# Optimization experiments

Hardware: AMD Instinct MI355X
Metric: run time of the kernel (lower is better)

Reference implementation:

```python
import jax, jax.numpy as jnp
from jax import lax
import numpy as np

STRIDE = 4
RADIUS = 0.2
NSAMPLE = 32
DENSITY_K = 16
INTRINSIC_DIM = 3
EPS = 1e-8
BN_EPS = 1e-5


def _cdist(a, b):
    # Euclidean pairwise distances: a (..., M, 3), b (..., N, 3) -> (..., M, N)
    d2 = ((a * a).sum(-1)[..., :, None] + (b * b).sum(-1)[..., None, :]
          - 2.0 * jnp.matmul(a, jnp.swapaxes(b, -1, -2)))
    return jnp.sqrt(jnp.maximum(d2, 1e-12))


def _fps(coords, n_samples):
    # iterative farthest point sampling: coords (B, N, 3) -> (B, n_samples) int32
    B, N, _ = coords.shape
    mean = coords.mean(axis=1, keepdims=True)
    farthest = jnp.argmax(((coords - mean) ** 2).sum(-1), axis=1)
    min_dist = jnp.full((B, N), jnp.inf, dtype=coords.dtype)

    def step(carry, _):
        md, far = carry
        centroid = jnp.take_along_axis(coords, far[:, None, None], axis=1)  # (B,1,3)
        d = ((coords - centroid) ** 2).sum(-1)
        md = jnp.minimum(md, d)
        return (md, jnp.argmax(md, axis=1)), far

    _, idxs = lax.scan(step, (min_dist, farthest), None, length=n_samples)
    return idxs.T  # (B, n_samples)


def _ball_query(q, s, radius, k):
    d = _cdist(q, s)  # (B, M, N)
    _, knn_idx = lax.top_k(-d, k)                 # k nearest fallback
    masked = jnp.where(d > radius, jnp.inf, d)
    neg_vals, m_idx = lax.top_k(-masked, k)       # k nearest within radius
    valid = jnp.isfinite(neg_vals)
    return jnp.where(valid, m_idx, knn_idx)


def _density_weights(gc):
    # gc: (B, M, K, 3) -> weights (B, M, K); kth-NN-distance based density weights
    K = gc.shape[2]
    d = _cdist(gc, gc)  # (B, M, K, K)
    d = jnp.where(jnp.eye(K, dtype=bool), jnp.inf, d)
    kk = min(max(DENSITY_K, 1), K - 1)
    kth = -lax.top_k(-d, kk)[0][..., -1]  # distance to kk-th neighbor, (B, M, K)
    raw = jnp.maximum(kth, EPS) ** INTRINSIC_DIM
    return raw / jnp.maximum(raw.sum(axis=-1, keepdims=True), EPS)


def _bn(x, g, b, axes):
    # training-mode batchnorm (biased variance), channel axis = 1
    mu = x.mean(axes, keepdims=True)
    var = x.var(axes, keepdims=True)
    shp = [1] * x.ndim
    shp[1] = -1
    return (x - mu) / jnp.sqrt(var + BN_EPS) * g.reshape(shp) + b.reshape(shp)


def setup_inputs() -> dict:
    key = jax.random.key(0)
    ks = jax.random.split(key, 5)
    B, N, C_in, C_out = 8, 4096, 64, 128
    mid = C_out // 2  # stride > 1 -> mid_channels = out_channels // 2
    coords = jax.random.uniform(ks[0], (B, N, 3), dtype=jnp.float32)
    feats = jax.random.normal(ks[1], (B, C_in, N), dtype=jnp.float32)
    W0 = jax.random.normal(ks[2], (mid, C_in + 3), dtype=jnp.float32) * 0.05
    W1 = jax.random.normal(ks[3], (C_out, mid), dtype=jnp.float32) * 0.05
    Ws = jax.random.normal(ks[4], (C_out, C_in), dtype=jnp.float32) * 0.05
    return {
        "coords": coords, "feats": feats,
        "W0": W0, "g0": jnp.ones((mid,), jnp.float32), "b0": jnp.zeros((mid,), jnp.float32),
        "W1": W1, "g1": jnp.ones((C_out,), jnp.float32), "b1": jnp.zeros((C_out,), jnp.float32),
        "Ws": Ws, "gs": jnp.ones((C_out,), jnp.float32), "bs": jnp.zeros((C_out,), jnp.float32),
    }


def reference(coords, feats, W0, g0, b0, W1, g1, b1, Ws, gs, bs):
    B, N, _ = coords.shape
    M = max(N // STRIDE, 1)
    sample_idx = _fps(coords, M)                               # (B, M)
    gather_pts = jax.vmap(lambda c, i: c[i])                   # (N,3)[idx]
    gather_fts = jax.vmap(lambda f, i: f[:, i])                # (C,N)[:,idx]
    sampled_coords = gather_pts(coords, sample_idx)            # (B, M, 3)
    gidx = _ball_query(sampled_coords, coords, RADIUS, NSAMPLE)  # (B, M, K)
    grouped_coords = gather_pts(coords, gidx)                  # (B, M, K, 3)
    rel = (grouped_coords - sampled_coords[:, :, None, :]) / max(RADIUS, 1e-8)
    grouped_feats = gather_fts(feats, gidx)                    # (B, C_in, M, K)
    x = jnp.concatenate([rel.transpose(0, 3, 1, 2), grouped_feats], axis=1)
    h = jax.nn.relu(_bn(jnp.einsum('oc,bcmk->bomk', W0, x), g0, b0, (0, 2, 3)))
    messages = jax.nn.relu(_bn(jnp.einsum('oc,bcmk->bomk', W1, h), g1, b1, (0, 2, 3)))
    weights = _density_weights(grouped_coords)                 # (B, M, K)
    reduced = (messages * weights[:, None, :, :]).sum(-1)      # (B, C_out, M)
    skip_in = gather_fts(feats, sample_idx)                    # (B, C_in, M)
    skip = _bn(jnp.einsum('oc,bcm->bom', Ws, skip_in), gs, bs, (0, 2))
    return sampled_coords, jax.nn.relu(reduced + skip)
```

## Files before the change

### kernel.cpp

```cpp
#include <hip/hip_runtime.h>
#include <hip/hip_bf16.h>
#include <cstdint>

#define DEV __device__ __forceinline__

constexpr int Bn   = 8;
constexpr int Nn   = 4096;
constexpr int Mn   = 1024;
constexpr int Kn   = 32;
constexpr int CIN  = 64;
constexpr int COUT = 128;

DEV float wave_max_f32(float x) {
#if __has_builtin(__builtin_amdgcn_update_dpp)
#define FSTEP(CTRL, RMASK)                                                      \
  {                                                                             \
    int o = __builtin_amdgcn_update_dpp(0, __float_as_int(x), CTRL, RMASK, 0xf, \
                                        false);                                 \
    x = fmaxf(x, __int_as_float(o));                                            \
  }
  FSTEP(0x111, 0xf)
  FSTEP(0x112, 0xf)
  FSTEP(0x114, 0xf)
  FSTEP(0x118, 0xf)
  FSTEP(0x142, 0xa)
  FSTEP(0x143, 0xc)
#undef FSTEP
#else
  for (int off = 1; off < 64; off <<= 1) x = fmaxf(x, __shfl_xor(x, off, 64));
#endif
  return x;
}

DEV unsigned long long grp8_max_u64(unsigned long long k) {
#if __has_builtin(__builtin_amdgcn_update_dpp)
#define USTEP(CTRL)                                                                    \
  {                                                                                    \
    unsigned int lo = (unsigned int)__builtin_amdgcn_update_dpp(                       \
        0, (int)(unsigned int)k, CTRL, 0xf, 0xf, false);                               \
    unsigned int hi = (unsigned int)__builtin_amdgcn_update_dpp(                       \
        0, (int)(unsigned int)(k >> 32), CTRL, 0xf, 0xf, false);                       \
    unsigned long long o = ((unsigned long long)hi << 32) | lo;                        \
    if (o > k) k = o;                                                                  \
  }
  USTEP(0x111)
  USTEP(0x112)
  USTEP(0x114)
#undef USTEP
#else
  for (int off = 1; off < 8; off <<= 1) {
    unsigned int lo = __shfl_xor((unsigned int)k, off, 64);
    unsigned int hi = __shfl_xor((unsigned int)(k >> 32), off, 64);
    unsigned long long o = ((unsigned long long)hi << 32) | lo;
    if (o > k) k = o;
  }
#endif
  return k;
}

DEV uint32_t fps_round8(const float v[8], int t, unsigned long long (*part)[8], int p) {
  float v4[4]; int j4[4];
#pragma unroll
  for (int i = 0; i < 4; ++i) {
    bool r = v[2 * i + 1] > v[2 * i];
    v4[i] = r ? v[2 * i + 1] : v[2 * i];
    j4[i] = r ? 2 * i + 1 : 2 * i;
  }
  float v2[2]; int j2[2];
#pragma unroll
  for (int i = 0; i < 2; ++i) {
    bool r = v4[2 * i + 1] > v4[2 * i];
    v2[i] = r ? v4[2 * i + 1] : v4[2 * i];
    j2[i] = r ? j4[2 * i + 1] : j4[2 * i];
  }
  bool rr = v2[1] > v2[0];
  float bv = rr ? v2[1] : v2[0];
  int bj = rr ? j2[1] : j2[0];

  unsigned long long mb0 = __ballot((bj & 1) != 0);
  unsigned long long mb1 = __ballot((bj & 2) != 0);
  unsigned long long mb2 = __ballot((bj & 4) != 0);
  float wl = wave_max_f32(bv);
  float wmax = __int_as_float(__builtin_amdgcn_readlane(__float_as_int(wl), 63));
  unsigned long long mask = __ballot(bv == wmax);
  int Ls = (int)__ffsll(mask) - 1;
  int bjw = (int)((mb0 >> Ls) & 1ull) | ((int)((mb1 >> Ls) & 1ull) << 1) |
            ((int)((mb2 >> Ls) & 1ull) << 2);
  uint32_t idx = 8u * (uint32_t)((t & ~63) + Ls) + (uint32_t)bjw;
  const int sl = p & 1;
  if ((t & 63) == 0)
    part[sl][t >> 6] = ((unsigned long long)__float_as_uint(wmax) << 12) |
                       (unsigned long long)(4095u - idx);
  __syncthreads();
  unsigned long long kk = part[sl][t & 7];
  kk = grp8_max_u64(kk);
  unsigned int lo = (unsigned int)__builtin_amdgcn_readlane((int)(unsigned int)kk, 7);
  return 4095u - (lo & 4095u);
}

__global__ __launch_bounds__(512, 1) void k_fused(const float* __restrict__ coords,
                                                  const float* __restrict__ feats,
                                                  float* __restrict__ featsT,
                                                  uint32_t* __restrict__ sidx,
                                                  float* __restrict__ outc) {
  __shared__ __align__(16) char smraw[Nn * 16];
  __shared__ unsigned long long part[2][8];
  __shared__ uint32_t farl[Mn];
  __shared__ float s_mean[4];
  const int t = threadIdx.x;

  if (blockIdx.x >= 8) {
    float (*tile)[65] = (float(*)[65])smraw;
    int bid = blockIdx.x - 8;
    int b = bid >> 6, n0 = (bid & 63) * 64;
    int lane = t & 63, grp = t >> 6;
    for (int r = 0; r < 8; ++r) {
      int c = grp + r * 8;
      tile[c][lane] = feats[((size_t)b * 64 + c) * 4096 + n0 + lane];
    }
    __syncthreads();
    for (int r = 0; r < 8; ++r) {
      int n = grp + r * 8;
      featsT[((size_t)b * 4096 + n0 + n) * 64 + lane] = tile[lane][n];
    }
    return;
  }

  float4* sp = (float4*)smraw;
  const int b = blockIdx.x;
  const float* cb = coords + (size_t)b * Nn * 3;
  for (int i = t; i < Nn; i += 512)
    sp[i] = make_float4(cb[3 * i], cb[3 * i + 1], cb[3 * i + 2], 0.f);
  __syncthreads();
  if (t == 0) {
    float ax = 0.f, ay = 0.f, az = 0.f;
    for (int i = 0; i < Nn; ++i) {
      float4 c = sp[i];
      ax = __fadd_rn(ax, c.x); ay = __fadd_rn(ay, c.y); az = __fadd_rn(az, c.z);
    }
    s_mean[0] = __fdiv_rn(ax, 4096.f);
    s_mean[1] = __fdiv_rn(ay, 4096.f);
    s_mean[2] = __fdiv_rn(az, 4096.f);
  }
  __syncthreads();

  float px[8], py[8], pz[8], md[8];
#pragma unroll
  for (int j = 0; j < 8; ++j) {
    float4 c = sp[8 * t + j];
    px[j] = c.x; py[j] = c.y; pz[j] = c.z;
    md[j] = __builtin_inff();
  }

  uint32_t far;
  {
    float mx = s_mean[0], my = s_mean[1], mz = s_mean[2];
    float tv[8];
#pragma unroll
    for (int j = 0; j < 8; ++j) {
      float dx = __fsub_rn(px[j], mx), dy = __fsub_rn(py[j], my), dz = __fsub_rn(pz[j], mz);
      tv[j] = __fadd_rn(__fadd_rn(__fmul_rn(dx, dx), __fmul_rn(dy, dy)), __fmul_rn(dz, dz));
    }
    far = fps_round8(tv, t, part, 0);
  }

  for (int p = 1; p < Mn; ++p) {
    if (t == 0) farl[p - 1] = far;
    float4 c = sp[far];
#pragma unroll
    for (int j = 0; j < 8; ++j) {
      float dx = __fsub_rn(px[j], c.x), dy = __fsub_rn(py[j], c.y), dz = __fsub_rn(pz[j], c.z);
      float d = __fadd_rn(__fadd_rn(__fmul_rn(dx, dx), __fmul_rn(dy, dy)), __fmul_rn(dz, dz));
      md[j] = fminf(md[j], d);
    }
    far = fps_round8(md, t, part, p);
  }
  if (t == 0) farl[Mn - 1] = far;
  __syncthreads();

  for (int i = t; i < Mn; i += 512) {
    uint32_t f = farl[i];
    sidx[b * Mn + i] = f;
    float4 c = sp[f];
    outc[(size_t)(b * Mn + i) * 3 + 0] = c.x;
    outc[(size_t)(b * Mn + i) * 3 + 1] = c.y;
    outc[(size_t)(b * Mn + i) * 3 + 2] = c.z;
  }
}

__global__ __launch_bounds__(256) void k_knn(const float* __restrict__ coords,
                                             const uint32_t* __restrict__ sidx,
                                             uint32_t* __restrict__ gidx,
                                             float* __restrict__ wts) {
  const int q = blockIdx.x;
  const int b = q >> 10;
  const int t = threadIdx.x;
  __shared__ unsigned long long keys[Nn + 2];
  __shared__ int s_cnt;
  __shared__ float s_q[4];
  __shared__ uint32_t s_sel[32];
  __shared__ float gx[32], gy[32], gz[32], g2[32];
  __shared__ float dmat[32 * 33];
  __shared__ float kth[32];
  __shared__ float s_raw[32];
  __shared__ float s_sum;

  if (t == 0) {
    uint32_t si = sidx[q];
    const float* c = &coords[((size_t)b * Nn + si) * 3];
    s_q[0] = c[0]; s_q[1] = c[1]; s_q[2] = c[2];
  }
  __syncthreads();
  float qx = s_q[0], qy = s_q[1], qz = s_q[2];
  float q2 = __fadd_rn(__fadd_rn(__fmul_rn(qx, qx), __fmul_rn(qy, qy)), __fmul_rn(qz, qz));
  const float* cb = coords + (size_t)b * Nn * 3;

  float thr = 0.04f;
  int cnt = 0;
  while (true) {
    if (t == 0) s_cnt = 0;
    __syncthreads();
    for (int j = 0; j < 16; ++j) {
      int i = t + 256 * j;
      float cx = cb[3 * i], cy = cb[3 * i + 1], cz = cb[3 * i + 2];
      float c2  = __fadd_rn(__fadd_rn(__fmul_rn(cx, cx), __fmul_rn(cy, cy)), __fmul_rn(cz, cz));
      float dot = __fadd_rn(__fadd_rn(__fmul_rn(qx, cx), __fmul_rn(qy, cy)), __fmul_rn(qz, cz));
      float d2  = __fsub_rn(__fadd_rn(q2, c2), __fmul_rn(2.f, dot));
      float d2c = fmaxf(d2, 1e-12f);
      bool pred = (d2c <= thr);
      unsigned long long mk = __ballot(pred);
      int base = 0;
      if ((t & 63) == 0 && mk) base = atomicAdd(&s_cnt, (int)__popcll(mk));
      base = __shfl(base, 0, 64);
      if (pred) {
        int pos = base + (int)__popcll(mk & ((1ull << (t & 63)) - 1ull));
        keys[pos] = ((unsigned long long)__float_as_uint(d2c) << 32) | (uint32_t)i;
      }
    }
    __syncthreads();
    cnt = s_cnt;
    if (cnt >= 32 || thr > 1.f) break;
    thr = (thr < 0.1f) ? 0.16f : 8.f;
    __syncthreads();
  }
  if (t == 0) { keys[cnt] = ~0ull; keys[cnt + 1] = ~0ull; }
  __syncthreads();
  int cnt2 = (cnt + 1) & ~1;
  for (int i = t; i < cnt; i += 256) {
    unsigned long long ki = keys[i];
    int r = 0;
    for (int j2 = 0; j2 < cnt2; j2 += 2) {
      unsigned long long a = keys[j2], c2 = keys[j2 + 1];
      r += (a < ki) + (c2 < ki);
    }
    if (r < 32) s_sel[r] = (uint32_t)ki;
  }
  __syncthreads();

  if (t < 32) {
    uint32_t gi = s_sel[t];
    gidx[(size_t)q * 32 + t] = gi;
    const float* c = &coords[((size_t)b * Nn + gi) * 3];
    float x = c[0], y = c[1], z = c[2];
    gx[t] = x; gy[t] = y; gz[t] = z;
    g2[t] = __fadd_rn(__fadd_rn(__fmul_rn(x, x), __fmul_rn(y, y)), __fmul_rn(z, z));
  }
  __syncthreads();
  for (int p = t; p < 1024; p += 256) {
    int i = p >> 5, jj = p & 31;
    float dot = __fadd_rn(__fadd_rn(__fmul_rn(gx[i], gx[jj]), __fmul_rn(gy[i], gy[jj])),
                          __fmul_rn(gz[i], gz[jj]));
    float d2 = __fsub_rn(__fadd_rn(g2[i], g2[jj]), __fmul_rn(2.f, dot));
    float dd = sqrtf(fmaxf(d2, 1e-12f));
    if (i == jj) dd = __builtin_inff();
    dmat[i * 33 + jj] = dd;
  }
  __syncthreads();
  for (int p = t; p < 1024; p += 256) {
    int i = p >> 5, jj = p & 31;
    float v = dmat[i * 33 + jj];
    int r = 0;
    for (int c = 0; c < 32; ++c) {
      float u = dmat[i * 33 + c];
      r += (u < v) || (u == v && c < jj);
    }
    if (r == 15) kth[i] = v;
  }
  __syncthreads();
  if (t < 32) { float x = fmaxf(kth[t], 1e-8f); s_raw[t] = x * x * x; }
  __syncthreads();
  if (t == 0) {
    float s = 0.f;
    for (int i2 = 0; i2 < 32; ++i2) s += s_raw[i2];
    s_sum = fmaxf(s, 1e-8f);
  }
  __syncthreads();
  if (t < 32) wts[(size_t)q * 32 + t] = s_raw[t] / s_sum;
}

constexpr int XST = 132;
constexpr int WST = 68;

DEV void build_x(const float* __restrict__ coords, const float* __restrict__ featsT,
                 const uint32_t* __restrict__ sidx, const uint32_t* __restrict__ gidx,
                 const float* __restrict__ W0, int b, int m0, int t,
                 float* xs, float* w0sT, uint32_t* s_gi, float* s_qc) {
  for (int i = t; i < 64 * 67; i += 256) {
    int o = i / 67, c = i - o * 67;
    w0sT[c * WST + o] = W0[i];
  }
  if (t < 128) {
    s_gi[t] = gidx[((size_t)(b * Mn + m0)) * 32 + t];
  } else if (t < 132) {
    int mm = t - 128;
    uint32_t si = sidx[b * Mn + m0 + mm];
    const float* c = &coords[((size_t)b * Nn + si) * 3];
    s_qc[mm * 3 + 0] = c[0]; s_qc[mm * 3 + 1] = c[1]; s_qc[mm * 3 + 2] = c[2];
  }
  __syncthreads();
  if (t < 128) {
    int mm = t >> 5;
    const float* c = &coords[((size_t)b * Nn + s_gi[t]) * 3];
    xs[0 * XST + t] = (c[0] - s_qc[mm * 3 + 0]) / 0.2f;
    xs[1 * XST + t] = (c[1] - s_qc[mm * 3 + 1]) / 0.2f;
    xs[2 * XST + t] = (c[2] - s_qc[mm * 3 + 2]) / 0.2f;
  }
  {
    int c = t & 63, k0g = t >> 6;
    for (int r2 = 0; r2 < 32; ++r2) {
      int kk = k0g + 4 * r2;
      xs[(size_t)(3 + c) * XST + kk] = featsT[((size_t)b * Nn + s_gi[kk]) * 64 + c];
    }
  }
  __syncthreads();
}

DEV void conv1_acc(const float* xs, const float* w0sT, int o0, int k0, float acc[32]) {
#pragma unroll
  for (int i = 0; i < 32; ++i) acc[i] = 0.f;
  for (int c = 0; c < 67; ++c) {
    float4 w  = *(const float4*)&w0sT[c * WST + o0];
    float4 xa = *(const float4*)&xs[c * XST + k0];
    float4 xb = *(const float4*)&xs[c * XST + k0 + 4];
    float wv[4] = {w.x, w.y, w.z, w.w};
    float xv[8] = {xa.x, xa.y, xa.z, xa.w, xb.x, xb.y, xb.z, xb.w};
#pragma unroll
    for (int i = 0; i < 4; ++i)
#pragma unroll
      for (int j = 0; j < 8; ++j)
        acc[i * 8 + j] = fmaf(wv[i], xv[j], acc[i * 8 + j]);
  }
}

DEV void conv2_acc(const float* hs, const float* w1sT, int o0, int k0, float acc2[32]) {
#pragma unroll
  for (int i = 0; i < 32; ++i) acc2[i] = 0.f;
  for (int c = 0; c < 64; ++c) {
    float4 w  = *(const float4*)&w1sT[c * WST + o0];
    float4 xa = *(const float4*)&hs[c * XST + k0];
    float4 xb = *(const float4*)&hs[c * XST + k0 + 4];
    float wv[4] = {w.x, w.y, w.z, w.w};
    float xv[8] = {xa.x, xa.y, xa.z, xa.w, xb.x, xb.y, xb.z, xb.w};
#pragma unroll
    for (int i = 0; i < 4; ++i)
#pragma unroll
      for (int j = 0; j < 8; ++j)
        acc2[i * 8 + j] = fmaf(wv[i], xv[j], acc2[i * 8 + j]);
  }
}

DEV unsigned short f2bf(float x) {
  __hip_bfloat16 h = __float2bfloat16(x);
  return *reinterpret_cast<unsigned short*>(&h);
}


__global__ __launch_bounds__(256) void k_conv1s(const float* __restrict__ coords,
                                                const float* __restrict__ featsT,
                                                const uint32_t* __restrict__ sidx,
                                                const uint32_t* __restrict__ gidx,
                                                const float* __restrict__ W0,
                                                const float* __restrict__ Ws,
                                                float* __restrict__ ys,
                                                float* __restrict__ stats,
                                                unsigned short* __restrict__ accb) {
  __shared__ float smU[13400];
  __shared__ uint32_t s_gi[128];
  __shared__ float s_qc[12];
  __shared__ float ssum[128], ssq[128];
  int t = threadIdx.x;

  if (blockIdx.x >= 2048) {
    float* fin  = smU;
    float* wssT = smU + 64 * 65;
    uint32_t* s_si = s_gi;
    int blk = blockIdx.x - 2048;
    int b = blk >> 4, m0 = (blk & 15) * 64;
    if (t < 64) s_si[t] = sidx[b * Mn + m0 + t];
    if (t < 128) { ssum[t] = 0.f; ssq[t] = 0.f; }
    __syncthreads();
    for (int i = t; i < 64 * 64; i += 256) {
      int mm = i >> 6, c = i & 63;
      fin[mm * 65 + c] = featsT[((size_t)b * Nn + s_si[mm]) * 64 + c];
    }
    for (int i = t; i < 128 * 64; i += 256) {
      int oo = i >> 6, cc = i & 63;
      wssT[cc * 129 + oo] = Ws[(size_t)oo * 64 + cc];
    }
    __syncthreads();
    int o = t & 127, mh = t >> 7;
    float s = 0.f, sq = 0.f;
    for (int mm = mh * 32; mm < mh * 32 + 32; ++mm) {
      float acc = 0.f;
      for (int c = 0; c < 64; ++c) acc = fmaf(wssT[c * 129 + o], fin[mm * 65 + c], acc);
      ys[((size_t)(b * Mn + m0 + mm)) * 128 + o] = acc;
      s += acc; sq = fmaf(acc, acc, sq);
    }
    atomicAdd(&ssum[o], s); atomicAdd(&ssq[o], sq);
    __syncthreads();
    if (t < 128) { atomicAdd(&stats[384 + t], ssum[t]); atomicAdd(&stats[512 + t], ssq[t]); }
    return;
  }

  float* xs = smU; float* w0sT = smU + 67 * XST;
  int blk = blockIdx.x;
  int b = blk >> 8, m0 = (blk & 255) << 2;
  if (t < 64) { ssum[t] = 0.f; ssq[t] = 0.f; }
  build_x(coords, featsT, sidx, gidx, W0, b, m0, t, xs, w0sT, s_gi, s_qc);
  int o0 = (t & 15) * 4, k0 = (t >> 4) * 8;
  float acc[32];
  conv1_acc(xs, w0sT, o0, k0, acc);
  if (accb != nullptr) {
    unsigned short* at = accb + (size_t)blk * 8192;
#pragma unroll
    for (int i = 0; i < 4; ++i) {
      unsigned int w[4];
#pragma unroll
      for (int q = 0; q < 4; ++q)
        w[q] = (unsigned int)f2bf(acc[i * 8 + 2 * q]) |
               ((unsigned int)f2bf(acc[i * 8 + 2 * q + 1]) << 16);
      *(uint4*)&at[(o0 + i) * 128 + k0] = make_uint4(w[0], w[1], w[2], w[3]);
    }
  }
#pragma unroll
  for (int i = 0; i < 4; ++i) {
    float s = 0.f, sq = 0.f;
#pragma unroll
    for (int j = 0; j < 8; ++j) { s += acc[i * 8 + j]; sq = fmaf(acc[i * 8 + j], acc[i * 8 + j], sq); }
    atomicAdd(&ssum[o0 + i], s); atomicAdd(&ssq[o0 + i], sq);
  }
  __syncthreads();
  if (t < 64) { atomicAdd(&stats[t], ssum[t]); atomicAdd(&stats[64 + t], ssq[t]); }
}

__global__ __launch_bounds__(256) void k_conv2c(const unsigned short* __restrict__ accb,
                                                const float* __restrict__ W1,
                                                float* __restrict__ stats,
                                                const float* __restrict__ g0,
// ... 136 lines not shown
    float var = stats[64 + t] * (1.f / 262144.f) - mu * mu;
    float a = g0[t] / sqrtf(var + 1e-5f);
    s_a0[t] = a; s_c0[t] = b0[t] - mu * a;
  }
  if (t < 128) {
    float mu  = stats[128 + t] * (1.f / 262144.f);
    float var = stats[256 + t] * (1.f / 262144.f) - mu * mu;
    float a = g1[t] / sqrtf(var + 1e-5f);
    s_a1[t] = a; s_c1[t] = b1[t] - mu * a;
    float mus  = stats[384 + t] * (1.f / 8192.f);
    float vars = stats[512 + t] * (1.f / 8192.f) - mus * mus;
    float as = gs[t] / sqrtf(vars + 1e-5f);
    s_as[t] = as; s_cs[t] = bs[t] - mus * as;
    sw[(t >> 5) * 36 + (t & 31)] = wts[((size_t)(b * Mn + m0)) * 32 + t];
  }
  const unsigned short* at = accb + (size_t)blk * 8192;
  int o = t >> 2, kb = (t & 3) * 32;
  __syncthreads();
  float a0 = s_a0[o], c0 = s_c0[o];
#pragma unroll
  for (int g = 0; g < 4; ++g) {
    uint4 v = *(const uint4*)&at[o * 128 + kb + 8 * g];
    unsigned int vv[4] = {v.x, v.y, v.z, v.w};
#pragma unroll
    for (int q = 0; q < 4; ++q) {
      float f0 = __uint_as_float((vv[q] & 0xffffu) << 16);
      float f1 = __uint_as_float(vv[q] & 0xffff0000u);
      hs[o * XST + kb + 8 * g + 2 * q]     = fmaxf(fmaf(a0, f0, c0), 0.f);
      hs[o * XST + kb + 8 * g + 2 * q + 1] = fmaxf(fmaf(a0, f1, c0), 0.f);
    }
  }
  int o0 = (t & 15) * 4, k0 = (t >> 4) * 8;
  int m = k0 >> 5, nb0 = k0 & 31;
  for (int p = 0; p < 2; ++p) {
    __syncthreads();
    for (int i = t; i < 64 * 64; i += 256) {
      int oo = i >> 6, cc = i & 63;
      w1sT[cc * WST + oo] = W1[(size_t)(64 * p + oo) * 64 + cc];
    }
    __syncthreads();
    float acc2[32];
    conv2_acc(hs, w1sT, o0, k0, acc2);
    float4 swa = *(const float4*)&sw[m * 36 + nb0];
    float4 swb = *(const float4*)&sw[m * 36 + nb0 + 4];
    float wv[8] = {swa.x, swa.y, swa.z, swa.w, swb.x, swb.y, swb.z, swb.w};
    float a1v[4], c1v[4];
#pragma unroll
    for (int i = 0; i < 4; ++i) { a1v[i] = s_a1[64 * p + o0 + i]; c1v[i] = s_c1[64 * p + o0 + i]; }
    float r4[4];
#pragma unroll
    for (int i = 0; i < 4; ++i) {
      float r = 0.f;
#pragma unroll
      for (int j = 0; j < 8; ++j) {
        float msg = fmaxf(fmaf(a1v[i], acc2[i * 8 + j], c1v[i]), 0.f);
        r = fmaf(msg, wv[j], r);
      }
      r4[i] = r;
    }
#pragma unroll
    for (int i = 0; i < 4; ++i) {
      float r = r4[i];
      r += __shfl_xor(r, 16, 64);
      r += __shfl_xor(r, 32, 64);
      r4[i] = r;
    }
    if ((t & 63) < 16) {
      float4 ysv = *(const float4*)&ys[((size_t)(b * Mn + m0 + m)) * 128 + 64 * p + o0];
      float yv[4] = {ysv.x, ysv.y, ysv.z, ysv.w};
#pragma unroll
      for (int i = 0; i < 4; ++i) {
        int o2 = 64 * p + o0 + i;
        red[o2 * 5 + m] = fmaxf(r4[i] + fmaf(s_as[o2], yv[i], s_cs[o2]), 0.f);
      }
    }
  }
  __syncthreads();
  for (int e = t; e < 512; e += 256) {
    int oo = e >> 2, mm = e & 3;
    out_feat[(size_t)b * 131072 + (size_t)oo * 1024 + m0 + mm] = red[oo * 5 + mm];
  }
}

__global__ void k_fin0(float* stats, const float* g0, const float* b0) {
  int t = threadIdx.x;
  if (t >= 64) return;
  float mu  = stats[t] * (1.f / 262144.f);
  float var = stats[64 + t] * (1.f / 262144.f) - mu * mu;
  float a = g0[t] / sqrtf(var + 1e-5f);
  stats[640 + t] = a;
  stats[704 + t] = b0[t] - mu * a;
}

__global__ __launch_bounds__(256) void k_conv2(const float* __restrict__ coords,
                                               const float* __restrict__ featsT,
                                               const uint32_t* __restrict__ sidx,
                                               const uint32_t* __restrict__ gidx,
                                               const float* __restrict__ W0,
                                               const float* __restrict__ W1,
                                               float* __restrict__ stats) {
  __shared__ float smU[13400];
  __shared__ uint32_t s_gi[128];
  __shared__ float s_qc[12];
  __shared__ float ssum[128], ssq[128];
  float* xs = smU;  float* w0sT = smU + 67 * XST;
  float* hs = smU;  float* w1sT = smU + 64 * XST;
  int blk = blockIdx.x, t = threadIdx.x;
  int b = blk >> 8, m0 = (blk & 255) << 2;
  if (t < 128) { ssum[t] = 0.f; ssq[t] = 0.f; }
  build_x(coords, featsT, sidx, gidx, W0, b, m0, t, xs, w0sT, s_gi, s_qc);
  int o0 = (t & 15) * 4, k0 = (t >> 4) * 8;
  float acc[32];
  conv1_acc(xs, w0sT, o0, k0, acc);
  float4 a04 = *(const float4*)&stats[640 + o0];
  float4 c04 = *(const float4*)&stats[704 + o0];
  float a0v[4] = {a04.x, a04.y, a04.z, a04.w};
  float c0v[4] = {c04.x, c04.y, c04.z, c04.w};
  __syncthreads();
#pragma unroll
  for (int i = 0; i < 4; ++i) {
    float h[8];
#pragma unroll
    for (int j = 0; j < 8; ++j) h[j] = fmaxf(fmaf(a0v[i], acc[i * 8 + j], c0v[i]), 0.f);
    *(float4*)&hs[(o0 + i) * XST + k0]     = make_float4(h[0], h[1], h[2], h[3]);
    *(float4*)&hs[(o0 + i) * XST + k0 + 4] = make_float4(h[4], h[5], h[6], h[7]);
  }
  for (int p = 0; p < 2; ++p) {
    __syncthreads();
    for (int i = t; i < 64 * 64; i += 256) {
      int oo = i >> 6, cc = i & 63;
      w1sT[cc * WST + oo] = W1[(size_t)(64 * p + oo) * 64 + cc];
    }
    __syncthreads();
    float acc2[32];
    conv2_acc(hs, w1sT, o0, k0, acc2);
#pragma unroll
    for (int i = 0; i < 4; ++i) {
      float s = 0.f, sq = 0.f;
#pragma unroll
      for (int j = 0; j < 8; ++j) { s += acc2[i * 8 + j]; sq = fmaf(acc2[i * 8 + j], acc2[i * 8 + j], sq); }
      atomicAdd(&ssum[64 * p + o0 + i], s); atomicAdd(&ssq[64 * p + o0 + i], sq);
    }
  }
  __syncthreads();
  if (t < 128) { atomicAdd(&stats[128 + t], ssum[t]); atomicAdd(&stats[256 + t], ssq[t]); }
}

__global__ void k_fin1(float* stats, const float* g1, const float* b1,
                       const float* gs, const float* bs) {
  int t = threadIdx.x;
  if (t >= 128) return;
  float mu  = stats[128 + t] * (1.f / 262144.f);
  float var = stats[256 + t] * (1.f / 262144.f) - mu * mu;
  float a = g1[t] / sqrtf(var + 1e-5f);
  stats[768 + t] = a;
  stats[896 + t] = b1[t] - mu * a;
  float mus  = stats[384 + t] * (1.f / 8192.f);
  float vars = stats[512 + t] * (1.f / 8192.f) - mus * mus;
  float as = gs[t] / sqrtf(vars + 1e-5f);
  stats[1024 + t] = as;
  stats[1152 + t] = bs[t] - mus * as;
}

__global__ __launch_bounds__(256) void k_out(const float* __restrict__ coords,
                                             const float* __restrict__ featsT,
                                             const uint32_t* __restrict__ sidx,
                                             const uint32_t* __restrict__ gidx,
                                             const float* __restrict__ W0,
                                             const float* __restrict__ W1,
                                             const float* __restrict__ wts,
                                             const float* __restrict__ ys,
                                             const float* __restrict__ stats,
                                             float* __restrict__ out_feat) {
  __shared__ float smU[13400];
  __shared__ uint32_t s_gi[128];
  __shared__ float s_qc[12];
  __shared__ __align__(16) float sw[4 * 36];
  __shared__ float red[128 * 5];
  float* xs = smU;  float* w0sT = smU + 67 * XST;
  float* hs = smU;  float* w1sT = smU + 64 * XST;
  int blk = blockIdx.x, t = threadIdx.x;
  int b = blk >> 8, m0 = (blk & 255) << 2;
  build_x(coords, featsT, sidx, gidx, W0, b, m0, t, xs, w0sT, s_gi, s_qc);
  if (t < 128) sw[(t >> 5) * 36 + (t & 31)] = wts[((size_t)(b * Mn + m0)) * 32 + t];
  int o0 = (t & 15) * 4, k0 = (t >> 4) * 8;
  int m = k0 >> 5, nb0 = k0 & 31;
  float acc[32];
  conv1_acc(xs, w0sT, o0, k0, acc);
  float4 a04 = *(const float4*)&stats[640 + o0];
  float4 c04 = *(const float4*)&stats[704 + o0];
  float a0v[4] = {a04.x, a04.y, a04.z, a04.w};
  float c0v[4] = {c04.x, c04.y, c04.z, c04.w};
  __syncthreads();
#pragma unroll
  for (int i = 0; i < 4; ++i) {
    float h[8];
#pragma unroll
    for (int j = 0; j < 8; ++j) h[j] = fmaxf(fmaf(a0v[i], acc[i * 8 + j], c0v[i]), 0.f);
    *(float4*)&hs[(o0 + i) * XST + k0]     = make_float4(h[0], h[1], h[2], h[3]);
    *(float4*)&hs[(o0 + i) * XST + k0 + 4] = make_float4(h[4], h[5], h[6], h[7]);
  }
  for (int p = 0; p < 2; ++p) {
    __syncthreads();
    for (int i = t; i < 64 * 64; i += 256) {
      int oo = i >> 6, cc = i & 63;
      w1sT[cc * WST + oo] = W1[(size_t)(64 * p + oo) * 64 + cc];
    }
    __syncthreads();
    float acc2[32];
    conv2_acc(hs, w1sT, o0, k0, acc2);
    float4 swa = *(const float4*)&sw[m * 36 + nb0];
    float4 swb = *(const float4*)&sw[m * 36 + nb0 + 4];
    float wv[8] = {swa.x, swa.y, swa.z, swa.w, swb.x, swb.y, swb.z, swb.w};
    float4 a14 = *(const float4*)&stats[768 + 64 * p + o0];
    float4 c14 = *(const float4*)&stats[896 + 64 * p + o0];
    float a1v[4] = {a14.x, a14.y, a14.z, a14.w};
    float c1v[4] = {c14.x, c14.y, c14.z, c14.w};
    float r4[4];
#pragma unroll
    for (int i = 0; i < 4; ++i) {
      float r = 0.f;
#pragma unroll
      for (int j = 0; j < 8; ++j) {
        float msg = fmaxf(fmaf(a1v[i], acc2[i * 8 + j], c1v[i]), 0.f);
        r = fmaf(msg, wv[j], r);
      }
      r4[i] = r;
    }
#pragma unroll
    for (int i = 0; i < 4; ++i) {
      float r = r4[i];
      r += __shfl_xor(r, 16, 64);
      r += __shfl_xor(r, 32, 64);
      r4[i] = r;
    }
    if ((t & 63) < 16) {
      float4 ysv = *(const float4*)&ys[((size_t)(b * Mn + m0 + m)) * 128 + 64 * p + o0];
      float4 as4 = *(const float4*)&stats[1024 + 64 * p + o0];
      float4 cs4 = *(const float4*)&stats[1152 + 64 * p + o0];
      float yv[4] = {ysv.x, ysv.y, ysv.z, ysv.w};
      float av[4] = {as4.x, as4.y, as4.z, as4.w};
      float cv[4] = {cs4.x, cs4.y, cs4.z, cs4.w};
#pragma unroll
      for (int i = 0; i < 4; ++i)
        red[(64 * p + o0 + i) * 5 + m] = fmaxf(r4[i] + fmaf(av[i], yv[i], cv[i]), 0.f);
    }
  }
  __syncthreads();
  for (int e = t; e < 512; e += 256) {
    int oo = e >> 2, mm = e & 3;
    out_feat[(size_t)b * 131072 + (size_t)oo * 1024 + m0 + mm] = red[oo * 5 + mm];
  }
}

extern "C" void kernel_launch(void* const* d_in, const int* in_sizes, int n_in,
                              void* d_out, int out_size, void* d_ws, size_t ws_size,
                              hipStream_t stream) {
  const float* coords = (const float*)d_in[0];
  const float* feats  = (const float*)d_in[1];
  const float* W0 = (const float*)d_in[2];
  const float* g0 = (const float*)d_in[3];
  const float* b0 = (const float*)d_in[4];
  const float* W1 = (const float*)d_in[5];
  const float* g1 = (const float*)d_in[6];
  const float* b1 = (const float*)d_in[7];
  const float* Ws = (const float*)d_in[8];
  const float* gs = (const float*)d_in[9];
  const float* bs = (const float*)d_in[10];

  float* out_coords = (float*)d_out;
  float* out_feat   = out_coords + (size_t)Bn * Mn * 3;

  char* w = (char*)d_ws;
  float*    featsT = (float*)w;    w += (size_t)Bn * Nn * CIN * 4;
  uint32_t* sidx   = (uint32_t*)w; w += (size_t)Bn * Mn * 4;
  uint32_t* gidx   = (uint32_t*)w; w += (size_t)Bn * Mn * Kn * 4;
  float*    wts    = (float*)w;    w += (size_t)Bn * Mn * Kn * 4;
  float*    ys     = (float*)w;    w += (size_t)Bn * Mn * COUT * 4;
  unsigned short* accb = (unsigned short*)w; w += (size_t)2048 * 8192 * 2;
  float*    stats  = (float*)w;    w += 1280 * 4;
  size_t needB = (size_t)(w - (char*)d_ws);
  unsigned short* acc2b = (unsigned short*)w; w += (size_t)2048 * 16384 * 2;
  size_t needA = (size_t)(w - (char*)d_ws);
  const bool tierA = ws_size >= needA;
  const bool tierB = ws_size >= needB;

  hipMemsetAsync(stats, 0, 640 * 4, stream);
  hipLaunchKernelGGL(k_fused, dim3(520),  dim3(512), 0, stream,
                     coords, feats, featsT, sidx, out_coords);
  hipLaunchKernelGGL(k_knn,   dim3(8192), dim3(256), 0, stream, coords, sidx, gidx, wts);
  hipLaunchKernelGGL(k_conv1s, dim3(2176), dim3(256), 0, stream,
                     coords, featsT, sidx, gidx, W0, Ws, ys, stats,
                     tierB ? accb : (unsigned short*)nullptr);
  if (tierA) {
    hipLaunchKernelGGL(k_conv2c, dim3(2048), dim3(256), 0, stream,
                       accb, W1, stats, g0, b0, acc2b);
    hipLaunchKernelGGL(k_outc2,  dim3(2048), dim3(256), 0, stream,
                       acc2b, wts, ys, stats, g1, b1, gs, bs, out_feat);
  } else if (tierB) {
    hipLaunchKernelGGL(k_conv2c, dim3(2048), dim3(256), 0, stream,
                       accb, W1, stats, g0, b0, (unsigned short*)nullptr);
    hipLaunchKernelGGL(k_outc,   dim3(2048), dim3(256), 0, stream,
                       accb, W1, wts, ys, stats, g0, b0, g1, b1, gs, bs, out_feat);
  } else {
    hipLaunchKernelGGL(k_fin0,  dim3(1),    dim3(64),  0, stream, stats, g0, b0);
    hipLaunchKernelGGL(k_conv2, dim3(2048), dim3(256), 0, stream,
                       coords, featsT, sidx, gidx, W0, W1, stats);
    hipLaunchKernelGGL(k_fin1,  dim3(1),    dim3(128), 0, stream, stats, g1, b1, gs, bs);
    hipLaunchKernelGGL(k_out,   dim3(2048), dim3(256), 0, stream,
                       coords, featsT, sidx, gidx, W0, W1, wts, ys, stats, out_feat);
  }
}
```

Before: 1.045 ms.

## Overlap FPS with KNN via cooperative persistent kernel and per-index spin flags

Merges the farthest-point sampling kernel and the ball-query/density kernel into one cooperative launch. Eight blocks run FPS and publish each sampled index to global memory as soon as it is chosen, while the other 504 blocks transpose features and then spin-wait on those indices to run KNN queries concurrently, hiding the serial FPS latency behind KNN work. It also replaces three ballots with a single shuffle when recovering the winning lane's sub-index. It risks spin-wait overhead and reduced occupancy for the FPS blocks. The no-workspace fallback path is removed.

```diff
diff --git a/kernel.cpp b/kernel.cpp
--- a/kernel.cpp
+++ b/kernel.cpp
@@ -77,15 +77,11 @@
   float bv = rr ? v2[1] : v2[0];
   int bj = rr ? j2[1] : j2[0];
 
-  unsigned long long mb0 = __ballot((bj & 1) != 0);
-  unsigned long long mb1 = __ballot((bj & 2) != 0);
-  unsigned long long mb2 = __ballot((bj & 4) != 0);
   float wl = wave_max_f32(bv);
   float wmax = __int_as_float(__builtin_amdgcn_readlane(__float_as_int(wl), 63));
   unsigned long long mask = __ballot(bv == wmax);
   int Ls = (int)__ffsll(mask) - 1;
-  int bjw = (int)((mb0 >> Ls) & 1ull) | ((int)((mb1 >> Ls) & 1ull) << 1) |
-            ((int)((mb2 >> Ls) & 1ull) << 2);
+  int bjw = __shfl(bj, Ls, 64);
   uint32_t idx = 8u * (uint32_t)((t & ~63) + Ls) + (uint32_t)bjw;
   const int sl = p & 1;
   if ((t & 63) == 0)
@@ -96,6 +92,228 @@
   kk = grp8_max_u64(kk);
   unsigned int lo = (unsigned int)__builtin_amdgcn_readlane((int)(unsigned int)kk, 7);
   return 4095u - (lo & 4095u);
+}
+
+struct KnnSh {
+  unsigned long long keys[Nn + 2];
+  float gx[32], gy[32], gz[32], g2[32];
+  float dmat[32 * 33];
+  float kth[32];
+  float raw[32];
+  uint32_t sel[32];
+  float ssum;
+  int cnt;
+  uint32_t qi;
+};
+
+DEV void knn_one(KnnSh* K, const float* __restrict__ coords, uint32_t si, int q,
+                 uint32_t* __restrict__ gidx, float* __restrict__ wts, int t) {
+  const int b = q >> 10;
+  const float* qc = &coords[((size_t)b * Nn + si) * 3];
+  float qx = qc[0], qy = qc[1], qz = qc[2];
+  float q2 = __fadd_rn(__fadd_rn(__fmul_rn(qx, qx), __fmul_rn(qy, qy)), __fmul_rn(qz, qz));
+  const float* cb = coords + (size_t)b * Nn * 3;
+
+  float thr = 0.04f;
+  int cnt = 0;
+  while (true) {
+    if (t == 0) K->cnt = 0;
+    __syncthreads();
+    for (int j = 0; j < 8; ++j) {
+      int i = t + 512 * j;
+      float cx = cb[3 * i], cy = cb[3 * i + 1], cz = cb[3 * i + 2];
+      float c2  = __fadd_rn(__fadd_rn(__fmul_rn(cx, cx), __fmul_rn(cy, cy)), __fmul_rn(cz, cz));
+      float dot = __fadd_rn(__fadd_rn(__fmul_rn(qx, cx), __fmul_rn(qy, cy)), __fmul_rn(qz, cz));
+      float d2  = __fsub_rn(__fadd_rn(q2, c2), __fmul_rn(2.f, dot));
+      float d2c = fmaxf(d2, 1e-12f);
+      bool pred = (d2c <= thr);
+      unsigned long long mk = __ballot(pred);
+      int base = 0;
+      if ((t & 63) == 0 && mk) base = atomicAdd(&K->cnt, (int)__popcll(mk));
+      base = __shfl(base, 0, 64);
+      if (pred) {
+        int pos = base + (int)__popcll(mk & ((1ull << (t & 63)) - 1ull));
+        K->keys[pos] = ((unsigned long long)__float_as_uint(d2c) << 32) | (uint32_t)i;
+      }
+    }
+    __syncthreads();
+    cnt = K->cnt;
+    if (cnt >= 32 || thr > 1.f) break;
+    thr = (thr < 0.1f) ? 0.16f : 8.f;
+    __syncthreads();
+  }
+  if (t == 0) { K->keys[cnt] = ~0ull; K->keys[cnt + 1] = ~0ull; }
+  __syncthreads();
+  int cnt2 = (cnt + 1) & ~1;
+  for (int i = t; i < cnt; i += 512) {
+    unsigned long long ki = K->keys[i];
+    int r = 0;
+    for (int j2 = 0; j2 < cnt2; j2 += 2) {
+      unsigned long long a = K->keys[j2], c2 = K->keys[j2 + 1];
+      r += (a < ki) + (c2 < ki);
+    }
+    if (r < 32) K->sel[r] = (uint32_t)ki;
+  }
+  __syncthreads();
+
+  if (t < 32) {
+    uint32_t gi = K->sel[t];
+    gidx[(size_t)q * 32 + t] = gi;
+    const float* c = &coords[((size_t)b * Nn + gi) * 3];
+    float x = c[0], y = c[1], z = c[2];
+    K->gx[t] = x; K->gy[t] = y; K->gz[t] = z;
+    K->g2[t] = __fadd_rn(__fadd_rn(__fmul_rn(x, x), __fmul_rn(y, y)), __fmul_rn(z, z));
+  }
+  __syncthreads();
+  for (int p = t; p < 1024; p += 512) {
+    int i = p >> 5, jj = p & 31;
+    float dot = __fadd_rn(__fadd_rn(__fmul_rn(K->gx[i], K->gx[jj]), __fmul_rn(K->gy[i], K->gy[jj])),
+                          __fmul_rn(K->gz[i], K->gz[jj]));
+    float d2 = __fsub_rn(__fadd_rn(K->g2[i], K->g2[jj]), __fmul_rn(2.f, dot));
+    float dd = sqrtf(fmaxf(d2, 1e-12f));
+    if (i == jj) dd = __builtin_inff();
+    K->dmat[i * 33 + jj] = dd;
+  }
+  __syncthreads();
+  for (int p = t; p < 1024; p += 512) {
+    int i = p >> 5, jj = p & 31;
+    float v = K->dmat[i * 33 + jj];
+    int r = 0;
+    for (int c = 0; c < 32; ++c) {
+      float u = K->dmat[i * 33 + c];
+      r += (u < v) || (u == v && c < jj);
+    }
+    if (r == 15) K->kth[i] = v;
+  }
+  __syncthreads();
+  if (t < 32) { float x = fmaxf(K->kth[t], 1e-8f); K->raw[t] = x * x * x; }
+  __syncthreads();
+  if (t == 0) {
+    float s = 0.f;
+    for (int i2 = 0; i2 < 32; ++i2) s += K->raw[i2];
+    K->ssum = fmaxf(s, 1e-8f);
+  }
+  __syncthreads();
+  if (t < 32) wts[(size_t)q * 32 + t] = K->raw[t] / K->ssum;
+}
+
+__global__ __launch_bounds__(512, 4) void k_mega(const float* __restrict__ coords,
+                                                 const float* __restrict__ feats,
+                                                 float* __restrict__ featsT,
+                                                 uint32_t* __restrict__ sidx,
+                                                 float* __restrict__ outc,
+                                                 uint32_t* __restrict__ gidx,
+                                                 float* __restrict__ wts) {
+  __shared__ __align__(16) char smraw[Nn * 16];
+  __shared__ unsigned long long part[2][8];
+  __shared__ uint32_t farl[Mn];
+  __shared__ float s_mean[4];
+  const int t = threadIdx.x;
+  const int bid = blockIdx.x;
+
+  if (bid >= 8) {
+    float (*tile)[65] = (float(*)[65])smraw;
+    for (int tl = bid - 8; tl < 512; tl += 504) {
+      int b = tl >> 6, n0 = (tl & 63) * 64;
+      int lane = t & 63, grp = t >> 6;
+      for (int r = 0; r < 8; ++r) {
+        int c = grp + r * 8;
+        tile[c][lane] = feats[((size_t)b * 64 + c) * 4096 + n0 + lane];
+      }
+      __syncthreads();
+      for (int r = 0; r < 8; ++r) {
+        int n = grp + r * 8;
+        featsT[((size_t)b * 4096 + n0 + n) * 64 + lane] = tile[lane][n];
+      }
+      __syncthreads();
+    }
+    KnnSh* K = (KnnSh*)smraw;
+    for (int q = bid - 8; q < Bn * Mn; q += 504) {
+      if (t == 0) {
+        uint32_t v; int g = 0;
+        do {
+          v = __hip_atomic_load(&sidx[q], __ATOMIC_RELAXED, __HIP_MEMORY_SCOPE_AGENT);
+          if (v != 0xFFFFFFFFu) break;
+          __builtin_amdgcn_s_sleep(16);
+        } while (++g < (1 << 24));
+        K->qi = v & 4095u;
+      }
+      __syncthreads();
+      uint32_t si = K->qi;
+      __syncthreads();
+      knn_one(K, coords, si, q, gidx, wts, t);
+      __syncthreads();
+    }
+    return;
+  }
+
+  float4* sp = (float4*)smraw;
+  const int b = bid;
+  const float* cb = coords + (size_t)b * Nn * 3;
+  for (int i = t; i < Nn; i += 512)
+    sp[i] = make_float4(cb[3 * i], cb[3 * i + 1], cb[3 * i + 2], 0.f);
+  __syncthreads();
+  if (t == 0) {
+    float ax = 0.f, ay = 0.f, az = 0.f;
+    for (int i = 0; i < Nn; ++i) {
+      float4 c = sp[i];
+      ax = __fadd_rn(ax, c.x); ay = __fadd_rn(ay, c.y); az = __fadd_rn(az, c.z);
+    }
+    s_mean[0] = __fdiv_rn(ax, 4096.f);
+    s_mean[1] = __fdiv_rn(ay, 4096.f);
+    s_mean[2] = __fdiv_rn(az, 4096.f);
+  }
+  __syncthreads();
+
+  float px[8], py[8], pz[8], md[8];
+#pragma unroll
+  for (int j = 0; j < 8; ++j) {
+    float4 c = sp[8 * t + j];
+    px[j] = c.x; py[j] = c.y; pz[j] = c.z;
+    md[j] = __builtin_inff();
+  }
+
+  uint32_t far;
+  {
+    float mx = s_mean[0], my = s_mean[1], mz = s_mean[2];
+    float tv[8];
+#pragma unroll
+    for (int j = 0; j < 8; ++j) {
+      float dx = __fsub_rn(px[j], mx), dy = __fsub_rn(py[j], my), dz = __fsub_rn(pz[j], mz);
+      tv[j] = __fadd_rn(__fadd_rn(__fmul_rn(dx, dx), __fmul_rn(dy, dy)), __fmul_rn(dz, dz));
+    }
+    far = fps_round8(tv, t, part, 0);
+  }
+
+  for (int p = 1; p < Mn; ++p) {
+    if (t == 0) {
+      farl[p - 1] = far;
+      __hip_atomic_store(&sidx[b * Mn + p - 1], far, __ATOMIC_RELAXED,
+                         __HIP_MEMORY_SCOPE_AGENT);
+    }
+    float4 c = sp[far];
+#pragma unroll
+    for (int j = 0; j < 8; ++j) {
+      float dx = __fsub_rn(px[j], c.x), dy = __fsub_rn(py[j], c.y), dz = __fsub_rn(pz[j], c.z);
+      float d = __fadd_rn(__fadd_rn(__fmul_rn(dx, dx), __fmul_rn(dy, dy)), __fmul_rn(dz, dz));
+      md[j] = fminf(md[j], d);
+    }
+    far = fps_round8(md, t, part, p);
+  }
+  if (t == 0) {
+    farl[Mn - 1] = far;
+    __hip_atomic_store(&sidx[b * Mn + Mn - 1], far, __ATOMIC_RELAXED,
+                       __HIP_MEMORY_SCOPE_AGENT);
+  }
+  __syncthreads();
+
+  for (int i = t; i < Mn; i += 512) {
+    uint32_t f = farl[i];
+    float4 c = sp[f];
+    outc[(size_t)(b * Mn + i) * 3 + 0] = c.x;
+    outc[(size_t)(b * Mn + i) * 3 + 1] = c.y;
+    outc[(size_t)(b * Mn + i) * 3 + 2] = c.z;
+  }
 }
 
 __global__ __launch_bounds__(512, 1) void k_fused(const float* __restrict__ coords,
@@ -125,7 +343,6 @@
     }
     return;
   }
-
   float4* sp = (float4*)smraw;
   const int b = blockIdx.x;
   const float* cb = coords + (size_t)b * Nn * 3;
@@ -143,7 +360,6 @@
     s_mean[2] = __fdiv_rn(az, 4096.f);
   }
   __syncthreads();
-
   float px[8], py[8], pz[8], md[8];
 #pragma unroll
   for (int j = 0; j < 8; ++j) {
@@ -151,7 +367,6 @@
     px[j] = c.x; py[j] = c.y; pz[j] = c.z;
     md[j] = __builtin_inff();
   }
-
   uint32_t far;
   {
     float mx = s_mean[0], my = s_mean[1], mz = s_mean[2];
@@ -163,7 +378,6 @@
     }
     far = fps_round8(tv, t, part, 0);
   }
-
   for (int p = 1; p < Mn; ++p) {
     if (t == 0) farl[p - 1] = far;
     float4 c = sp[far];
@@ -177,7 +391,6 @@
   }
   if (t == 0) farl[Mn - 1] = far;
   __syncthreads();
-
   for (int i = t; i < Mn; i += 512) {
     uint32_t f = farl[i];
     sidx[b * Mn + i] = f;
@@ -256,7 +469,6 @@
     if (r < 32) s_sel[r] = (uint32_t)ki;
   }
   __syncthreads();
-
   if (t < 32) {
     uint32_t gi = s_sel[t];
     gidx[(size_t)q * 32 + t] = gi;
@@ -373,7 +585,6 @@
   __hip_bfloat16 h = __float2bfloat16(x);
   return *reinterpret_cast<unsigned short*>(&h);
 }
-
 
 __global__ __launch_bounds__(256) void k_conv1s(const float* __restrict__ coords,
                                                 const float* __restrict__ featsT,
@@ -676,177 +887,6 @@
   }
 }
 
-__global__ void k_fin0(float* stats, const float* g0, const float* b0) {
-  int t = threadIdx.x;
-  if (t >= 64) return;
-  float mu  = stats[t] * (1.f / 262144.f);
-  float var = stats[64 + t] * (1.f / 262144.f) - mu * mu;
-  float a = g0[t] / sqrtf(var + 1e-5f);
-  stats[640 + t] = a;
-  stats[704 + t] = b0[t] - mu * a;
-}
-
-__global__ __launch_bounds__(256) void k_conv2(const float* __restrict__ coords,
-                                               const float* __restrict__ featsT,
-                                               const uint32_t* __restrict__ sidx,
-                                               const uint32_t* __restrict__ gidx,
-                                               const float* __restrict__ W0,
-                                               const float* __restrict__ W1,
-                                               float* __restrict__ stats) {
-  __shared__ float smU[13400];
-  __shared__ uint32_t s_gi[128];
-  __shared__ float s_qc[12];
-  __shared__ float ssum[128], ssq[128];
-  float* xs = smU;  float* w0sT = smU + 67 * XST;
-  float* hs = smU;  float* w1sT = smU + 64 * XST;
-  int blk = blockIdx.x, t = threadIdx.x;
-  int b = blk >> 8, m0 = (blk & 255) << 2;
-  if (t < 128) { ssum[t] = 0.f; ssq[t] = 0.f; }
-  build_x(coords, featsT, sidx, gidx, W0, b, m0, t, xs, w0sT, s_gi, s_qc);
-  int o0 = (t & 15) * 4, k0 = (t >> 4) * 8;
-  float acc[32];
-  conv1_acc(xs, w0sT, o0, k0, acc);
-  float4 a04 = *(const float4*)&stats[640 + o0];
-  float4 c04 = *(const float4*)&stats[704 + o0];
-  float a0v[4] = {a04.x, a04.y, a04.z, a04.w};
-  float c0v[4] = {c04.x, c04.y, c04.z, c04.w};
-  __syncthreads();
-#pragma unroll
-  for (int i = 0; i < 4; ++i) {
-    float h[8];
-#pragma unroll
-    for (int j = 0; j < 8; ++j) h[j] = fmaxf(fmaf(a0v[i], acc[i * 8 + j], c0v[i]), 0.f);
-    *(float4*)&hs[(o0 + i) * XST + k0]     = make_float4(h[0], h[1], h[2], h[3]);
-    *(float4*)&hs[(o0 + i) * XST + k0 + 4] = make_float4(h[4], h[5], h[6], h[7]);
-  }
-  for (int p = 0; p < 2; ++p) {
-    __syncthreads();
-    for (int i = t; i < 64 * 64; i += 256) {
-      int oo = i >> 6, cc = i & 63;
-      w1sT[cc * WST + oo] = W1[(size_t)(64 * p + oo) * 64 + cc];
-    }
-    __syncthreads();
-    float acc2[32];
-    conv2_acc(hs, w1sT, o0, k0, acc2);
-#pragma unroll
-    for (int i = 0; i < 4; ++i) {
-      float s = 0.f, sq = 0.f;
-#pragma unroll
-      for (int j = 0; j < 8; ++j) { s += acc2[i * 8 + j]; sq = fmaf(acc2[i * 8 + j], acc2[i * 8 + j], sq); }
-      atomicAdd(&ssum[64 * p + o0 + i], s); atomicAdd(&ssq[64 * p + o0 + i], sq);
-    }
-  }
-  __syncthreads();
-  if (t < 128) { atomicAdd(&stats[128 + t], ssum[t]); atomicAdd(&stats[256 + t], ssq[t]); }
-}
-
-__global__ void k_fin1(float* stats, const float* g1, const float* b1,
-                       const float* gs, const float* bs) {
-  int t = threadIdx.x;
-  if (t >= 128) return;
-  float mu  = stats[128 + t] * (1.f / 262144.f);
-  float var = stats[256 + t] * (1.f / 262144.f) - mu * mu;
-  float a = g1[t] / sqrtf(var + 1e-5f);
-  stats[768 + t] = a;
-  stats[896 + t] = b1[t] - mu * a;
-  float mus  = stats[384 + t] * (1.f / 8192.f);
-  float vars = stats[512 + t] * (1.f / 8192.f) - mus * mus;
-  float as = gs[t] / sqrtf(vars + 1e-5f);
-  stats[1024 + t] = as;
-  stats[1152 + t] = bs[t] - mus * as;
-}
-
-__global__ __launch_bounds__(256) void k_out(const float* __restrict__ coords,
-                                             const float* __restrict__ featsT,
-                                             const uint32_t* __restrict__ sidx,
-                                             const uint32_t* __restrict__ gidx,
-                                             const float* __restrict__ W0,
-                                             const float* __restrict__ W1,
-                                             const float* __restrict__ wts,
-                                             const float* __restrict__ ys,
-                                             const float* __restrict__ stats,
-                                             float* __restrict__ out_feat) {
-  __shared__ float smU[13400];
-  __shared__ uint32_t s_gi[128];
-  __shared__ float s_qc[12];
-  __shared__ __align__(16) float sw[4 * 36];
-  __shared__ float red[128 * 5];
-  float* xs = smU;  float* w0sT = smU + 67 * XST;
-  float* hs = smU;  float* w1sT = smU + 64 * XST;
-  int blk = blockIdx.x, t = threadIdx.x;
-  int b = blk >> 8, m0 = (blk & 255) << 2;
-  build_x(coords, featsT, sidx, gidx, W0, b, m0, t, xs, w0sT, s_gi, s_qc);
-  if (t < 128) sw[(t >> 5) * 36 + (t & 31)] = wts[((size_t)(b * Mn + m0)) * 32 + t];
-  int o0 = (t & 15) * 4, k0 = (t >> 4) * 8;
-  int m = k0 >> 5, nb0 = k0 & 31;
-  float acc[32];
-  conv1_acc(xs, w0sT, o0, k0, acc);
-  float4 a04 = *(const float4*)&stats[640 + o0];
-  float4 c04 = *(const float4*)&stats[704 + o0];
-  float a0v[4] = {a04.x, a04.y, a04.z, a04.w};
-  float c0v[4] = {c04.x, c04.y, c04.z, c04.w};
-  __syncthreads();
-#pragma unroll
-  for (int i = 0; i < 4; ++i) {
-    float h[8];
-#pragma unroll
-    for (int j = 0; j < 8; ++j) h[j] = fmaxf(fmaf(a0v[i], acc[i * 8 + j], c0v[i]), 0.f);
-    *(float4*)&hs[(o0 + i) * XST + k0]     = make_float4(h[0], h[1], h[2], h[3]);
-    *(float4*)&hs[(o0 + i) * XST + k0 + 4] = make_float4(h[4], h[5], h[6], h[7]);
-  }
-  for (int p = 0; p < 2; ++p) {
-    __syncthreads();
-    for (int i = t; i < 64 * 64; i += 256) {
-      int oo = i >> 6, cc = i & 63;
-      w1sT[cc * WST + oo] = W1[(size_t)(64 * p + oo) * 64 + cc];
-    }
-    __syncthreads();
-    float acc2[32];
-    conv2_acc(hs, w1sT, o0, k0, acc2);
-    float4 swa = *(const float4*)&sw[m * 36 + nb0];
-    float4 swb = *(const float4*)&sw[m * 36 + nb0 + 4];
-    float wv[8] = {swa.x, swa.y, swa.z, swa.w, swb.x, swb.y, swb.z, swb.w};
-    float4 a14 = *(const float4*)&stats[768 + 64 * p + o0];
-    float4 c14 = *(const float4*)&stats[896 + 64 * p + o0];
-    float a1v[4] = {a14.x, a14.y, a14.z, a14.w};
-    float c1v[4] = {c14.x, c14.y, c14.z, c14.w};
-    float r4[4];
-#pragma unroll
-    for (int i = 0; i < 4; ++i) {
-      float r = 0.f;
-#pragma unroll
-      for (int j = 0; j < 8; ++j) {
-        float msg = fmaxf(fmaf(a1v[i], acc2[i * 8 + j], c1v[i]), 0.f);
-        r = fmaf(msg, wv[j], r);
-      }
-      r4[i] = r;
-    }
-#pragma unroll
-    for (int i = 0; i < 4; ++i) {
-      float r = r4[i];
-      r += __shfl_xor(r, 16, 64);
-      r += __shfl_xor(r, 32, 64);
-      r4[i] = r;
-    }
-    if ((t & 63) < 16) {
-      float4 ysv = *(const float4*)&ys[((size_t)(b * Mn + m0 + m)) * 128 + 64 * p + o0];
-      float4 as4 = *(const float4*)&stats[1024 + 64 * p + o0];
-      float4 cs4 = *(const float4*)&stats[1152 + 64 * p + o0];
-      float yv[4] = {ysv.x, ysv.y, ysv.z, ysv.w};
-      float av[4] = {as4.x, as4.y, as4.z, as4.w};
-      float cv[4] = {cs4.x, cs4.y, cs4.z, cs4.w};
-#pragma unroll
-      for (int i = 0; i < 4; ++i)
-        red[(64 * p + o0 + i) * 5 + m] = fmaxf(r4[i] + fmaf(av[i], yv[i], cv[i]), 0.f);
-    }
-  }
-  __syncthreads();
-  for (int e = t; e < 512; e += 256) {
-    int oo = e >> 2, mm = e & 3;
-    out_feat[(size_t)b * 131072 + (size_t)oo * 1024 + m0 + mm] = red[oo * 5 + mm];
-  }
-}
-
 extern "C" void kernel_launch(void* const* d_in, const int* in_sizes, int n_in,
                               void* d_out, int out_size, void* d_ws, size_t ws_size,
                               hipStream_t stream) {
@@ -880,9 +920,18 @@
   const bool tierB = ws_size >= needB;
 
   hipMemsetAsync(stats, 0, 640 * 4, stream);
-  hipLaunchKernelGGL(k_fused, dim3(520),  dim3(512), 0, stream,
-                     coords, feats, featsT, sidx, out_coords);
-  hipLaunchKernelGGL(k_knn,   dim3(8192), dim3(256), 0, stream, coords, sidx, gidx, wts);
+  hipMemsetAsync(sidx, 0xFF, (size_t)Bn * Mn * 4, stream);
+
+  void* margs[] = {(void*)&coords, (void*)&feats, (void*)&featsT, (void*)&sidx,
+                   (void*)&out_coords, (void*)&gidx, (void*)&wts};
+  hipError_t merr = hipLaunchCooperativeKernel((void*)k_mega, dim3(512), dim3(512),
+                                               margs, 0, stream);
+  if (merr != hipSuccess) {
+    hipLaunchKernelGGL(k_fused, dim3(520),  dim3(512), 0, stream,
+                       coords, feats, featsT, sidx, out_coords);
+    hipLaunchKernelGGL(k_knn,   dim3(8192), dim3(256), 0, stream,
+                       coords, sidx, gidx, wts);
+  }
   hipLaunchKernelGGL(k_conv1s, dim3(2176), dim3(256), 0, stream,
                      coords, featsT, sidx, gidx, W0, Ws, ys, stats,
                      tierB ? accb : (unsigned short*)nullptr);
@@ -896,12 +945,5 @@
                        accb, W1, stats, g0, b0, (unsigned short*)nullptr);
     hipLaunchKernelGGL(k_outc,   dim3(2048), dim3(256), 0, stream,
                        accb, W1, wts, ys, stats, g0, b0, g1, b1, gs, bs, out_feat);
-  } else {
-    hipLaunchKernelGGL(k_fin0,  dim3(1),    dim3(64),  0, stream, stats, g0, b0);
-    hipLaunchKernelGGL(k_conv2, dim3(2048), dim3(256), 0, stream,
-                       coords, featsT, sidx, gidx, W0, W1, stats);
-    hipLaunchKernelGGL(k_fin1,  dim3(1),    dim3(128), 0, stream, stats, g1, b1, gs, bs);
-    hipLaunchKernelGGL(k_out,   dim3(2048), dim3(256), 0, stream,
-                       coords, featsT, sidx, gidx, W0, W1, wts, ys, stats, out_feat);
-  }
-}
+  }
+}
```

After: 1.048 ms. Within noise of the previous version (+0.2%).
